# Kernel optimization log

Measured on AMD Instinct MI355X. Metric: run time of the kernel, lower is better.

Reference implementation:

```python
import jax, jax.numpy as jnp
import numpy as np
from jax import lax

T, B = 32, 16
NUM_ACTIONS = 18
HID = 256
C_V, C_K, C_S, NQ = 120, 8, 64, 4
NKEY, NVAL = C_K + C_S, C_V + C_S
Hh, Ww = 27, 20


def _spatial_basis():
    # Fourier spatial basis from Mott et al.; U = V = 8 -> 64 channels.
    h, w, U = Hh, Ww, 8
    p_h = np.arange(1, h + 1)[:, None] * np.ones((1, w)) * (np.pi / h)
    p_w = np.ones((h, 1)) * np.arange(1, w + 1)[None, :] * (np.pi / w)
    u = np.arange(1, U + 1)
    a = np.cos(p_h[:, :, None] * u)  # (h,w,8)
    b = np.cos(p_w[:, :, None] * u)  # (h,w,8)
    S = np.einsum('hwu,hwv->hwuv', a, b).reshape(h, w, U * U)
    return jnp.asarray(S, jnp.float32)

_S = _spatial_basis()


def _conv(x, w, b, stride, pad):
    y = lax.conv_general_dilated(x, w, stride, pad,
                                 dimension_numbers=('NCHW', 'OIHW', 'NCHW'))
    return y + b[None, :, None, None]


def setup_inputs() -> dict:
    key = jax.random.key(0)
    ks = iter(jax.random.split(key, 40))
    f32 = jnp.float32
    def rn(shape, s=0.05):
        return jax.random.normal(next(ks), shape, dtype=f32) * s
    return dict(
        frame=jax.random.normal(next(ks), (T, B, 3, 210, 160), dtype=f32),
        done=jnp.zeros((T, B), dtype=bool),
        last_action=jax.random.randint(next(ks), (T, B), 0, NUM_ACTIONS),
        reward=jax.random.normal(next(ks), (T, B), dtype=f32),
        core_h=jnp.zeros((B, HID), f32), core_c=jnp.zeros((B, HID), f32),
        conv_h=jnp.zeros((B, HID // 2, Hh, Ww), f32),
        conv_c=jnp.zeros((B, HID // 2, Hh, Ww), f32),
        cnn_w1=rn((32, 3, 8, 8)), cnn_b1=rn((32,)),
        cnn_w2=rn((64, 32, 4, 4)), cnn_b2=rn((64,)),
        lstm_w=rn((512, 192, 3, 3)), lstm_b=rn((512,)),
        qw1=rn((HID, 128)), qb1=rn((128,)),
        qw2=rn((128, NQ * NKEY)), qb2=rn((NQ * NKEY,)),
        qw3=rn((NQ * NKEY, NQ * NKEY)), qb3=rn((NQ * NKEY,)),
        aw1=rn((NVAL * NQ + NKEY * NQ + 1 + NUM_ACTIONS, 2 * HID)), ab1=rn((2 * HID,)),
        aw2=rn((2 * HID, HID)), ab2=rn((HID,)),
        w_ih=rn((4 * HID, HID)), w_hh=rn((4 * HID, HID)),
        b_ih=rn((4 * HID,)), b_hh=rn((4 * HID,)),
        pw=rn((HID, NUM_ACTIONS)), pb=rn((NUM_ACTIONS,)),
        vw=rn((HID, 1)), vb=rn((1,)),
    )


def reference(frame, done, last_action, reward, core_h, core_c, conv_h, conv_c,
              cnn_w1, cnn_b1, cnn_w2, cnn_b2, lstm_w, lstm_b,
              qw1, qb1, qw2, qb2, qw3, qb3, aw1, ab1, aw2, ab2,
              w_ih, w_hh, b_ih, b_hh, pw, pb, vw, vb):
    x = frame.reshape(T * B, 3, 210, 160)
    x = _conv(x, cnn_w1, cnn_b1, (4, 4), [(1, 1), (2, 2)])
    x = _conv(x, cnn_w2, cnn_b2, (2, 2), [(2, 2), (1, 1)])  # (T*B,64,27,20)
    x = x.reshape(T, B, 64, Hh, Ww)
    nd = (~done).astype(jnp.float32)  # (T,B)

    def vis_step(carry, inp):
        h, c = carry
        x_t, nd_t = inp
        m = nd_t[:, None, None, None]
        h, c = m * h, m * c
        gates = _conv(jnp.concatenate([x_t, h], axis=1), lstm_w, lstm_b,
                      (1, 1), [(1, 1), (1, 1)])
        ai, af, ao, ag = jnp.split(gates, 4, axis=1)
        c = jax.nn.sigmoid(af) * c + jax.nn.sigmoid(ai) * jnp.tanh(ag)
        h = jax.nn.sigmoid(ao) * jnp.tanh(c)
        return (h, c), h

    (vh, vc), O = lax.scan(vis_step, (conv_h, conv_c), (x, nd))
    # Faithful to the original `.view(N, h, w, c)` (a reinterpret, not a transpose).
    O = O.reshape(T * B, Hh, Ww, 128)
    Sb = jnp.broadcast_to(_S, (T * B, Hh, Ww, C_S))
    K = jnp.concatenate([O[..., :C_K], Sb], axis=3).reshape(T, B, Hh, Ww, NKEY)
    V = jnp.concatenate([O[..., C_K:], Sb], axis=3).reshape(T, B, Hh, Ww, NVAL)

    a1h = jax.nn.one_hot(last_action, NUM_ACTIONS, dtype=jnp.float32)  # (T,B,A)
    r = jnp.clip(reward, -1.0, 1.0)[..., None]  # (T,B,1)

    def core_step(carry, inp):
        h, c = carry
        K_t, V_t, r_t, a_t, nd_t = inp
        q = jax.nn.relu(h @ qw1 + qb1)
        q = jax.nn.relu(q @ qw2 + qb2)
        q = (q @ qw3 + qb3).reshape(B, NQ, NKEY)
        A = jnp.einsum('bhwk,bqk->bhwq', K_t, q)
        A = jax.nn.softmax(A.reshape(B, Hh * Ww, NQ), axis=1).reshape(B, Hh, Ww, NQ)
        ans = jnp.einsum('bhwq,bhwv->bqv', A, V_t)  # (B,NQ,NVAL)
        answer = jnp.concatenate(
            [ans.reshape(B, -1), q.reshape(B, -1), r_t, a_t], axis=1)
        ci = jax.nn.relu(answer @ aw1 + ab1) @ aw2 + ab2
        m = nd_t[:, None]
        h, c = m * h, m * c
        gates = ci @ w_ih.T + b_ih + h @ w_hh.T + b_hh  # torch gate order i,f,g,o
        gi, gf, gg, go = jnp.split(gates, 4, axis=1)
        c = jax.nn.sigmoid(gf) * c + jax.nn.sigmoid(gi) * jnp.tanh(gg)
        h = jax.nn.sigmoid(go) * jnp.tanh(c)
        return (h, c), h

    (ch, cc), outs = lax.scan(core_step, (core_h, core_c), (K, V, r, a1h, nd))
    out = outs.reshape(T * B, HID)
    logits = out @ pw + pb
    values = out @ vw + vb
    action = jnp.argmax(logits, axis=1)  # eval-mode action selection
    return (logits.reshape(T, B, NUM_ACTIONS), values.reshape(T, B),
            action.reshape(T, B), ch, cc, vh, vc)
```

## Files before the change

kernel.cpp:

```cpp
#include <hip/hip_runtime.h>
#include <math.h>

#define T_ 32
#define B_ 16
#define NA 18
#define P_ 540

typedef __attribute__((ext_vector_type(8)))  short short8;
typedef __attribute__((ext_vector_type(16))) float f32x16;

__device__ __forceinline__ float sigm(float x){ return 1.0f/(1.0f+expf(-x)); }
__device__ __forceinline__ unsigned short f2bf(float f){
    unsigned u = __float_as_uint(f);
    u += 0x7fff + ((u>>16)&1u);
    return (unsigned short)(u>>16);
}
__device__ __forceinline__ float bfu(unsigned short u){ return __uint_as_float(((unsigned)u)<<16); }

__global__ __launch_bounds__(256) void conv1k(const float* __restrict__ frame,
                                              const float* __restrict__ w,
                                              const float* __restrict__ bias,
                                              unsigned short* __restrict__ c1pad){
    __shared__ float tile[6048];
    int bid = blockIdx.x;
    int n = bid / 26, oh = (bid % 26)*2;
    int tid = threadIdx.x;
    const float* fb = frame + (size_t)n*3*210*160;
    for (int s = tid; s < 6048; s += 256){
        int col = s % 168;
        int row = (s/168) % 12;
        int ic  = s / 2016;
        int iy = oh*4 - 1 + row;
        int ix = col - 2;
        float v = 0.f;
        if (iy >= 0 && iy < 210 && ix >= 0 && ix < 160) v = fb[ic*33600 + iy*160 + ix];
        tile[s] = v;
    }
    __syncthreads();
    int oc = tid & 31, grp = tid >> 5;
    float acc[10] = {0.f,0.f,0.f,0.f,0.f,0.f,0.f,0.f,0.f,0.f};
    const float* wb = w + oc*192;
    for (int ic=0; ic<3; ++ic){
        #pragma unroll
        for (int kh=0; kh<8; ++kh){
            const float* wr = wb + ic*64 + kh*8;
            float4 w0 = *((const float4*)wr);
            float4 w1 = *((const float4*)(wr+4));
            const float* rowA = tile + ic*2016 + kh*168 + grp*20;
            float r[24];
            *((float4*)(r+ 0)) = *((const float4*)(rowA+ 0));
            *((float4*)(r+ 4)) = *((const float4*)(rowA+ 4));
            *((float4*)(r+ 8)) = *((const float4*)(rowA+ 8));
            *((float4*)(r+12)) = *((const float4*)(rowA+12));
            *((float4*)(r+16)) = *((const float4*)(rowA+16));
            *((float4*)(r+20)) = *((const float4*)(rowA+20));
            #pragma unroll
            for (int o=0;o<5;++o){
                acc[o] += r[o*4+0]*w0.x + r[o*4+1]*w0.y + r[o*4+2]*w0.z + r[o*4+3]*w0.w
                        + r[o*4+4]*w1.x + r[o*4+5]*w1.y + r[o*4+6]*w1.z + r[o*4+7]*w1.w;
            }
            const float* rowB = rowA + 672;
            *((float4*)(r+ 0)) = *((const float4*)(rowB+ 0));
            *((float4*)(r+ 4)) = *((const float4*)(rowB+ 4));
            *((float4*)(r+ 8)) = *((const float4*)(rowB+ 8));
            *((float4*)(r+12)) = *((const float4*)(rowB+12));
            *((float4*)(r+16)) = *((const float4*)(rowB+16));
            *((float4*)(r+20)) = *((const float4*)(rowB+20));
            #pragma unroll
            for (int o=0;o<5;++o){
                acc[5+o] += r[o*4+0]*w0.x + r[o*4+1]*w0.y + r[o*4+2]*w0.z + r[o*4+3]*w0.w
                          + r[o*4+4]*w1.x + r[o*4+5]*w1.y + r[o*4+6]*w1.z + r[o*4+7]*w1.w;
            }
        }
    }
    float bi = bias[oc];
    unsigned short* ob = c1pad + ((size_t)(n*32 + oc)*56 + oh+2)*42 + 1;
    #pragma unroll
    for (int o=0;o<5;++o) ob[grp*5+o] = f2bf(acc[o] + bi);
    ob += 42;
    #pragma unroll
    for (int o=0;o<5;++o) ob[grp*5+o] = f2bf(acc[5+o] + bi);
}

__global__ void apack2k(const float* __restrict__ w2, unsigned short* __restrict__ ap){
    int idx = blockIdx.x*256 + threadIdx.x;
    if (idx >= 32768) return;
    int j = idx & 7;
    int lane = (idx>>3) & 63;
    int mt = (idx>>9) & 1;
    int ic = idx >> 10;
    int k = ((lane>>5)<<3) + j;
    int oc = mt*32 + (lane & 31);
    ap[idx] = f2bf(w2[((oc*32 + ic)<<4) + k]);
}

__global__ __launch_bounds__(256) void c2mfma(const unsigned short* __restrict__ c1pad,
                                              const unsigned short* __restrict__ apack2,
                                              const float* __restrict__ bias,
                                              unsigned short* __restrict__ xpad){
    __shared__ unsigned short p2[2][3072];
    __shared__ float bsm[64];
    int bid = blockIdx.x;
    int s = bid / 5;
    int n0 = (bid % 5) * 128;
    int tid = threadIdx.x;
    int wave = tid >> 6, lane = tid & 63;
    int khalf = (lane>>5) << 3;
    if (tid < 64) bsm[tid] = bias[tid];
    const unsigned short* cb = c1pad + (size_t)s*32*2352;

    int soff[8], swaddr[8];
    #pragma unroll
    for (int q=0;q<8;++q){
        int idx = q*256 + tid;
        int n = idx & 127, k = idx >> 7;
        int p = n0 + n; if (p > 539) p = 539;
        soff[q] = ((p/20)*2 + (k>>2))*42 + (p%20)*2 + (k&3);
        swaddr[q] = n*24 + k;
    }
    #pragma unroll
    for (int q=0;q<8;++q) p2[0][swaddr[q]] = cb[soff[q]];
    unsigned short rv[8];
    #pragma unroll
    for (int q=0;q<8;++q) rv[q] = cb[2352 + soff[q]];

    int mt = wave >> 1, ntb = (wave & 1) * 2;
    short8 acur = *((const short8*)(apack2 + ((size_t)mt*64 + lane)*8));
    short8 anxt;
    f32x16 acc[2];
    #pragma unroll
    for (int jj=0;jj<2;++jj)
        #pragma unroll
        for (int rg=0;rg<16;++rg) acc[jj][rg] = 0.f;
    __syncthreads();

    for (int c=0; c<32; ++c){
        int buf = c & 1;
        if (c < 31){
            #pragma unroll
            for (int q=0;q<8;++q) p2[buf^1][swaddr[q]] = rv[q];
        }
        if (c < 30){
            const unsigned short* src = cb + (size_t)(c+2)*2352;
            #pragma unroll
            for (int q=0;q<8;++q) rv[q] = src[soff[q]];
        }
        if (c < 31) anxt = *((const short8*)(apack2 + ((size_t)((c+1)*2 + mt)*64 + lane)*8));
        #pragma unroll
        for (int jj=0;jj<2;++jj){
            int n = (ntb+jj)*32 + (lane & 31);
            short8 bf = *((const short8*)(&p2[buf][n*24 + khalf]));
            acc[jj] = __builtin_amdgcn_mfma_f32_32x32x16_bf16(acur, bf, acc[jj], 0, 0, 0);
        }
        acur = anxt;
        __syncthreads();
    }
    #pragma unroll
    for (int jj=0;jj<2;++jj){
        int pos = n0 + (ntb+jj)*32 + (lane & 31);
        if (pos >= 540) continue;
        int y = pos/20, x = pos%20;
        unsigned short* op = xpad + (size_t)s*64*640 + (y+1)*22 + x + 1;
        #pragma unroll
        for (int rg=0; rg<16; ++rg){
            int oc = mt*32 + (rg & 3) + 8*(rg>>2) + 4*(lane>>5);
            op[(size_t)oc*640] = f2bf(acc[jj][rg] + bsm[oc]);
        }
    }
}

__global__ void sbasisk(float* __restrict__ S){
    int idx = blockIdx.x*256 + threadIdx.x;
    if (idx >= P_*64) return;
    int s = idx & 63, p = idx >> 6;
    int y = p/20, x = p%20;
    int u = s >> 3, v = s & 7;
    double a  = cos((double)((y+1)*(u+1)) * M_PI / 27.0);
    double bb = cos((double)((x+1)*(v+1)) * M_PI / 20.0);
    S[idx] = (float)(a*bb);
}

__global__ void packw4k(const float* __restrict__ in, unsigned short* __restrict__ out, int R, int C){
    int idx = blockIdx.x*256 + threadIdx.x;
    int r4cnt = (R+3)>>2;
    if (idx >= r4cnt*C*4) return;
    int j = idx & 3;
    int rc = idx >> 2;
    int c = rc % C;
    int r = (rc / C)*4 + j;
    out[idx] = (r < R) ? f2bf(in[(size_t)r*C + c]) : (unsigned short)0;
}
__global__ void packt4k(const float* __restrict__ in, unsigned short* __restrict__ out, int R, int C){
    int idx = blockIdx.x*256 + threadIdx.x;
    int r4cnt = (R+3)>>2;
    if (idx >= r4cnt*C*4) return;
    int j = idx & 3;
    int rc = idx >> 2;
    int c = rc % C;
    int r = (rc / C)*4 + j;
    out[idx] = (r < R) ? f2bf(in[(size_t)c*R + r]) : (unsigned short)0;
}

__global__ void apack9k(const float* __restrict__ lw, unsigned short* __restrict__ ap){
    int idx = blockIdx.x*256 + threadIdx.x;
    if (idx >= 884736) return;
    int j = idx & 7;
    int lane = (idx>>3) & 63;
    int mt = (idx>>9) & 15;
    int f  = idx >> 13;
    int tap = f / 12, c = f % 12;
    int ch = c*16 + ((lane>>5)<<3) + j;
    int oc = mt*32 + (lane & 31);
    ap[idx] = f2bf(lw[(size_t)oc*1728 + ch*9 + tap]);
}

__global__ void h0packk(const float* __restrict__ h0, unsigned short* __restrict__ hpad){
    int idx = blockIdx.x*256 + threadIdx.x;
    if (idx >= 16*128*540) return;
    int plane = idx / 540, p = idx % 540;
    hpad[(size_t)plane*640 + (p/20+1)*22 + (p%20) + 1] = f2bf(h0[idx]);
}

__global__ __launch_bounds__(512) void gvck(const unsigned short* __restrict__ xpad,
                                            const unsigned short* __restrict__ hrd,
                                            unsigned short* __restrict__ hwr,
                                            const unsigned short* __restrict__ apack,
                                            const float* __restrict__ lb,
                                            const unsigned char* __restrict__ done,
                                            float* __restrict__ vh, float* __restrict__ vc,
                                            unsigned short* __restrict__ hreA,
                                            const float* __restrict__ S,
                                            const unsigned short* __restrict__ pq1, const float* __restrict__ qb1,
                                            const unsigned short* __restrict__ pq2, const float* __restrict__ qb2,
                                            const unsigned short* __restrict__ pq3, const float* __restrict__ qb3,
                                            const unsigned short* __restrict__ pa1, const float* __restrict__ ab1,
                                            const unsigned short* __restrict__ pa2, const float* __restrict__ ab2,
                                            const unsigned short* __restrict__ pih, const unsigned short* __restrict__ phh,
                                            const float* __restrict__ bih, const float* __restrict__ bhh,
                                            const float* __restrict__ reward, const int* __restrict__ lact,
                                            float* __restrict__ hsb, float* __restrict__ csb,
                                            float* __restrict__ outs,
                                            int t){
    __shared__ __align__(16) unsigned char smraw[65536];
    int bid = blockIdx.x;
    int tid = threadIdx.x;

    if (bid < 288){
        if (t >= T_) return;
        unsigned short* sm = (unsigned short*)smraw;
        float* gsm = (float*)smraw;
        int b  = bid % 16;
        int r  = bid / 16;
        int nb = r % 9;
        int mh = r / 9;
        int wave = tid >> 6, lane = tid & 63;
        int khalf = (lane>>5) << 3;
        int n0 = nb * 64;
        int y0 = n0 / 20;
        bool dn = done[t*B_ + b];

        const unsigned short* xb = xpad + ((size_t)(t*B_ + b))*64*640;
        const unsigned short* hb = hrd + (size_t)b*128*640;

        for (int rr = tid; rr < 1152; rr += 512){
            int ch = rr / 6, r6 = rr % 6;
            int prow = y0 + r6;
            unsigned short* dst = sm + (r6*22)*200 + ch;
            if (prow <= 28 && !(dn && ch >= 64)){
                const unsigned short* srcp = (ch < 64) ? (xb + ch*640 + prow*22)
                                                       : (hb + (ch-64)*640 + prow*22);
                const unsigned int* s32 = (const unsigned int*)srcp;
                #pragma unroll
                for (int c2=0;c2<11;++c2){
                    unsigned int v = s32[c2];
                    dst[(2*c2)*200]   = (unsigned short)(v & 0xffffu);
                    dst[(2*c2+1)*200] = (unsigned short)(v >> 16);
                }
            } else {
                #pragma unroll
                for (int c2=0;c2<22;++c2) dst[c2*200] = 0;
            }
        }

        int mt = (wave>>1)*4 + mh*2 + (wave&1);
        int sb[2];
        #pragma unroll
        for (int jj=0;jj<2;++jj){
            int p = n0 + jj*32 + (lane & 31); if (p > 539) p = 539;
            sb[jj] = ((p/20) - y0)*22 + (p%20);
        }
        f32x16 acc[2];
        #pragma unroll
        for (int jj=0;jj<2;++jj)
            #pragma unroll
            for (int rg=0;rg<16;++rg) acc[jj][rg] = 0.f;
        __syncthreads();

        for (int tap=0; tap<9; ++tap){
            int tadd = (tap/3)*22 + (tap%3);
            #pragma unroll
            for (int c=0;c<12;++c){
                short8 af = *((const short8*)(apack + ((size_t)((tap*12+c)*16 + mt)*64 + lane)*8));
                int ch0 = c*16 + khalf;
                short8 b0 = *((const short8*)(&sm[(sb[0]+tadd)*200 + ch0]));
                short8 b1 = *((const short8*)(&sm[(sb[1]+tadd)*200 + ch0]));
                acc[0] = __builtin_amdgcn_mfma_f32_32x32x16_bf16(af, b0, acc[0], 0, 0, 0);
                acc[1] = __builtin_amdgcn_mfma_f32_32x32x16_bf16(af, b1, acc[1], 0, 0, 0);
            }
        }
        __syncthreads();

        int g8 = wave >> 1, ih = wave & 1;
        #pragma unroll
        for (int j=0;j<2;++j){
            int p_loc = j*32 + (lane & 31);
            #pragma unroll
            for (int rg=0; rg<16; ++rg){
                int c_loc = ih*32 + 4*(lane>>5) + (rg & 3) + 8*(rg>>2);
                gsm[g8*4096 + c_loc*64 + p_loc] = acc[j][rg];
            }
        }
        __syncthreads();

        {
            int p_loc = tid & 63, c0 = tid >> 6;
            int pg = n0 + p_loc;
            if (pg < 540){
                float m = dn ? 0.f : 1.f;
                int y = pg/20, x = pg%20;
                #pragma unroll
                for (int e=0;e<8;++e){
                    int c_loc = c0*8 + e;
                    int cg = mh*64 + c_loc;
                    float gi = gsm[        c_loc*64 + p_loc] + lb[      cg];
                    float gf = gsm[ 4096 + c_loc*64 + p_loc] + lb[128 + cg];
                    float go = gsm[ 8192 + c_loc*64 + p_loc] + lb[256 + cg];
                    float gg = gsm[12288 + c_loc*64 + p_loc] + lb[384 + cg];
                    size_t idx = ((size_t)b*128 + cg)*540 + pg;
                    float cold = vc[idx] * m;
                    float cn = sigm(gf)*cold + sigm(gi)*tanhf(gg);
                    float hn = sigm(go)*tanhf(cn);
                    vc[idx] = cn;
                    if (t == T_-1) vh[idx] = hn;
                    hwr[((size_t)b*128 + cg)*640 + (y+1)*22 + x + 1] = f2bf(hn);
                    int flat = cg*540 + pg;
                    int pos = (flat/2560)*20 + (flat/128)%20;
                    int ch  = flat & 127;
                    hreA[((size_t)(t*B_ + b)*540 + pos)*128 + ch] = f2bf(hn);
                }
            }
        }
        return;
    }

    if (t == 0) return;
    int tc = t - 1;
    int b = bid - 288;
    float* fs = (float*)smraw;
    float* hs   = fs;
    float* cs   = fs + 256;
    float* hs2  = fs + 512;
    float* q1   = fs + 768;
    float* q2   = fs + 896;
    float* q3   = fs + 1184;
    float* elog = fs + 1472;
    float* red  = fs + 3632;
    float* ansv = fs + 3664;
    float* hid  = fs + 4720;
    float* cis  = fs + 5232;
    float* gb   = fs + 5488;

    if (tid < 256){ hs[tid] = hsb[b*256+tid]; cs[tid] = csb[b*256+tid]; }
    if (tid >= 256 && tid < 269) ansv[1043 + (tid-256)] = 0.f;
    __syncthreads();

    float m = done[tc*B_+b] ? 0.f : 1.f;
    if (tid < 128){
        float a0=0.f,a1=0.f,a2=0.f,a3=0.f;
        for (int i4=0;i4<64;++i4){
            ushort4 w = *((const ushort4*)(pq1 + (size_t)((i4<<7)+tid)*4));
            float4 h4 = *((const float4*)(hs + i4*4));
            a0 += h4.x*bfu(w.x); a1 += h4.y*bfu(w.y);
            a2 += h4.z*bfu(w.z); a3 += h4.w*bfu(w.w);
        }
        q1[tid] = fmaxf(qb1[tid] + ((a0+a1)+(a2+a3)), 0.f);
    }
    __syncthreads();
    if (tid < 288){
        float a0=0.f,a1=0.f,a2=0.f,a3=0.f;
        for (int i4=0;i4<32;++i4){
            ushort4 w = *((const ushort4*)(pq2 + (size_t)(i4*288+tid)*4));
            float4 h4 = *((const float4*)(q1 + i4*4));
            a0 += h4.x*bfu(w.x); a1 += h4.y*bfu(w.y);
            a2 += h4.z*bfu(w.z); a3 += h4.w*bfu(w.w);
        }
        q2[tid] = fmaxf(qb2[tid] + ((a0+a1)+(a2+a3)), 0.f);
    }
    __syncthreads();
    if (tid < 288){
        float a0=0.f,a1=0.f,a2=0.f,a3=0.f;
        for (int i4=0;i4<72;++i4){
            ushort4 w = *((const ushort4*)(pq3 + (size_t)(i4*288+tid)*4));
            float4 h4 = *((const float4*)(q2 + i4*4));
            a0 += h4.x*bfu(w.x); a1 += h4.y*bfu(w.y);
            a2 += h4.z*bfu(w.z); a3 += h4.w*bfu(w.w);
        }
        float a = qb3[tid] + ((a0+a1)+(a2+a3));
        q3[tid] = a;
        ansv[736+tid] = a;
    }
    if (tid == 0){ float r = reward[tc*B_+b]; ansv[1024] = fminf(1.f,fmaxf(-1.f,r)); }
    if (tid >= 32 && tid < 32+NA) ansv[1025 + tid-32] = (lact[tc*B_+b] == tid-32) ? 1.f : 0.f;
    __syncthreads();

    const unsigned short* hrb = hreA + (size_t)(tc*B_ + b)*540*128;
    for (int idx = tid; idx < 4*P_; idx += 512){
        int qi = idx / P_, p = idx % P_;
        const unsigned short* hp = hrb + (size_t)p*128;
        uint4 hv = *((const uint4*)hp);
        const float* qv = q3 + qi*72;
        float a = __uint_as_float(hv.x<<16)*qv[0] + __uint_as_float(hv.x & 0xffff0000u)*qv[1]
                + __uint_as_float(hv.y<<16)*qv[2] + __uint_as_float(hv.y & 0xffff0000u)*qv[3]
                + __uint_as_float(hv.z<<16)*qv[4] + __uint_as_float(hv.z & 0xffff0000u)*qv[5]
                + __uint_as_float(hv.w<<16)*qv[6] + __uint_as_float(hv.w & 0xffff0000u)*qv[7];
        const float* Sp = S + p*64;
        #pragma unroll
        for (int s2=0;s2<16;++s2){
            float4 sv = *((const float4*)(Sp + 4*s2));
            a += sv.x*qv[8+4*s2] + sv.y*qv[9+4*s2] + sv.z*qv[10+4*s2] + sv.w*qv[11+4*s2];
        }
        elog[qi*P_ + p] = a;
    }
    __syncthreads();
    {
        int qi = tid >> 7, lt = tid & 127;
        float mx = -1e30f;
        for (int p = lt; p < P_; p += 128) mx = fmaxf(mx, elog[qi*P_ + p]);
        for (int off=32; off; off>>=1) mx = fmaxf(mx, __shfl_down(mx, off));
        if ((tid & 63) == 0) red[tid>>6] = mx;
        __syncthreads();
        if (tid < 4) red[16+tid] = fmaxf(red[2*tid], red[2*tid+1]);
        __syncthreads();
        mx = red[16+qi];
        float sm = 0.f;
        for (int p = lt; p < P_; p += 128){ float e = expf(elog[qi*P_ + p]-mx); elog[qi*P_ + p] = e; sm += e; }
        for (int off=32; off; off>>=1) sm += __shfl_down(sm, off);
        if ((tid & 63) == 0) red[8 + (tid>>6)] = sm;
        __syncthreads();
        if (tid < 4) red[24+tid] = red[8+2*tid] + red[8+2*tid+1];
        __syncthreads();
    }
    if (tid < 240){
        int g = tid >> 2;
        int qi = g / 15, vb = g % 15;
        int pc = tid & 3;
        float ac[8] = {0,0,0,0,0,0,0,0};
        const unsigned short* hb8 = hrb + 8 + vb*8;
        for (int p = pc*135; p < pc*135+135; ++p){
            float e = elog[qi*P_ + p];
            uint4 hv = *((const uint4*)(hb8 + (size_t)p*128));
            ac[0] += e*__uint_as_float(hv.x<<16);
            ac[1] += e*__uint_as_float(hv.x & 0xffff0000u);
            ac[2] += e*__uint_as_float(hv.y<<16);
            ac[3] += e*__uint_as_float(hv.y & 0xffff0000u);
            ac[4] += e*__uint_as_float(hv.z<<16);
            ac[5] += e*__uint_as_float(hv.z & 0xffff0000u);
            ac[6] += e*__uint_as_float(hv.w<<16);
            ac[7] += e*__uint_as_float(hv.w & 0xffff0000u);
        }
        #pragma unroll
        for (int j=0;j<8;++j){ ac[j] += __shfl_down(ac[j],2); ac[j] += __shfl_down(ac[j],1); }
        if ((tid&3)==0){
            float inv2 = 1.f/red[24+qi];
            #pragma unroll
            for (int j=0;j<8;++j) ansv[qi*184 + vb*8 + j] = ac[j]*inv2;
        }
    } else if (tid < 496){
        int u = tid - 240;
        int g = u >> 2;
        int qi = g >> 4, vb4 = g & 15;
        int pc = u & 3;
        float ac[4] = {0,0,0,0};
        const float* Sp = S + vb4*4;
        for (int p = pc*135; p < pc*135+135; ++p){
            float e = elog[qi*P_ + p];
            float4 sv = *((const float4*)(Sp + (size_t)p*64));
            ac[0]+=e*sv.x; ac[1]+=e*sv.y; ac[2]+=e*sv.z; ac[3]+=e*sv.w;
        }
        #pragma unroll
        for (int j=0;j<4;++j){ ac[j] += __shfl_down(ac[j],2); ac[j] += __shfl_down(ac[j],1); }
        if ((tid&3)==0){
            float inv2 = 1.f/red[24+qi];
            #pragma unroll
            for (int j=0;j<4;++j) ansv[qi*184 + 120 + vb4*4 + j] = ac[j]*inv2;
        }
    }
    __syncthreads();
    {
        float a0=ab1[tid], a1=0.f, a2=0.f, a3=0.f;
        for (int i4=0;i4<261;++i4){
            ushort4 w = *((const ushort4*)(pa1 + (size_t)((i4<<9)+tid)*4));
            float4 av = *((const float4*)(ansv + i4*4));
            a0 += av.x*bfu(w.x); a1 += av.y*bfu(w.y);
            a2 += av.z*bfu(w.z); a3 += av.w*bfu(w.w);
        }
        hid[tid] = fmaxf((a0+a1)+(a2+a3), 0.f);
    }
    if (tid < 256) hs2[tid] = hs[tid]*m;
    __syncthreads();
    if (tid < 256){
        float a0=ab2[tid],a1=0.f,a2=0.f,a3=0.f;
        for (int i4=0;i4<128;++i4){
            ushort4 w = *((const ushort4*)(pa2 + (size_t)((i4<<8)+tid)*4));
            float4 hv = *((const float4*)(hid + i4*4));
            a0 += hv.x*bfu(w.x); a1 += hv.y*bfu(w.y);
            a2 += hv.z*bfu(w.z); a3 += hv.w*bfu(w.w);
        }
        cis[tid] = (a0+a1)+(a2+a3);
    }
    __syncthreads();
    for (int g = tid; g < 1024; g += 512){
        float a0=bih[g]+bhh[g], a1=0.f, a2=0.f, a3=0.f;
        for (int i4=0;i4<64;++i4){
            ushort4 wi = *((const ushort4*)(pih + (size_t)((i4<<10)+g)*4));
            ushort4 wh = *((const ushort4*)(phh + (size_t)((i4<<10)+g)*4));
            float4 cv = *((const float4*)(cis + i4*4));
            float4 hv = *((const float4*)(hs2 + i4*4));
            a0 += cv.x*bfu(wi.x) + hv.x*bfu(wh.x);
            a1 += cv.y*bfu(wi.y) + hv.y*bfu(wh.y);
            a2 += cv.z*bfu(wi.z) + hv.z*bfu(wh.z);
            a3 += cv.w*bfu(wi.w) + hv.w*bfu(wh.w);
        }
        gb[g] = (a0+a1)+(a2+a3);
    }
    __syncthreads();
    if (tid < 256){
        float gi = gb[tid], gf = gb[256+tid], gg = gb[512+tid], go = gb[768+tid];
        float cold = cs[tid]*m;
        float cn = sigm(gf)*cold + sigm(gi)*tanhf(gg);
        float hn = sigm(go)*tanhf(cn);
        csb[b*256+tid] = cn;
        hsb[b*256+tid] = hn;
        outs[(tc*B_+b)*256+tid] = hn;
    }
}

__global__ __launch_bounds__(64) void finalk(const float* __restrict__ outs,
                                             const float* __restrict__ pw, const float* __restrict__ pb,
                                             const float* __restrict__ vw, const float* __restrict__ vb,
                                             float* __restrict__ dout){
    int row = blockIdx.x, tid = threadIdx.x;
    __shared__ float os[256];
    __shared__ float lg[NA];
    for (int i=tid; i<256; i+=64) os[i] = outs[row*256+i];
    __syncthreads();
    if (tid < NA){
        float a = pb[tid];
        for (int i=0;i<256;++i) a += os[i]*pw[i*NA+tid];
        lg[tid] = a;
        dout[row*NA + tid] = a;
    } else if (tid == 32){
        float a = vb[0];
        for (int i=0;i<256;++i) a += os[i]*vw[i];
        dout[9216 + row] = a;
    }
    __syncthreads();
    if (tid == 0){
        int am = 0; float bv = lg[0];
        for (int j=1;j<NA;++j) if (lg[j] > bv){ bv = lg[j]; am = j; }
        dout[9728 + row] = (float)am;
    }
}

extern "C" void kernel_launch(void* const* d_in, const int* in_sizes, int n_in,
                              void* d_out, int out_size, void* d_ws, size_t ws_size,
                              hipStream_t stream) {
    const float* frame   = (const float*)d_in[0];
    const unsigned char* done = (const unsigned char*)d_in[1];
    const int*   lact    = (const int*)d_in[2];
    const float* reward  = (const float*)d_in[3];
    const float* core_h0 = (const float*)d_in[4];
    const float* core_c0 = (const float*)d_in[5];
    const float* conv_h0 = (const float*)d_in[6];
    const float* conv_c0 = (const float*)d_in[7];
    const float* cnn_w1  = (const float*)d_in[8];
    const float* cnn_b1  = (const float*)d_in[9];
    const float* cnn_w2  = (const float*)d_in[10];
    const float* cnn_b2  = (const float*)d_in[11];
    const float* lstm_w  = (const float*)d_in[12];
    const float* lstm_b  = (const float*)d_in[13];
    const float* qw1 = (const float*)d_in[14]; const float* qb1 = (const float*)d_in[15];
    const float* qw2 = (const float*)d_in[16]; const float* qb2 = (const float*)d_in[17];
    const float* qw3 = (const float*)d_in[18]; const float* qb3 = (const float*)d_in[19];
    const float* aw1 = (const float*)d_in[20]; const float* ab1 = (const float*)d_in[21];
    const float* aw2 = (const float*)d_in[22]; const float* ab2 = (const float*)d_in[23];
    const float* w_ih = (const float*)d_in[24]; const float* w_hh = (const float*)d_in[25];
    const float* b_ih = (const float*)d_in[26]; const float* b_hh = (const float*)d_in[27];
    const float* pw = (const float*)d_in[28]; const float* pb = (const float*)d_in[29];
    const float* vw = (const float*)d_in[30]; const float* vb = (const float*)d_in[31];

    float* ws = (float*)d_ws;
    float* dout = (float*)d_out;

    unsigned short* xpad   = (unsigned short*)ws;
    unsigned short* c1pad  = (unsigned short*)(ws + 10485760);
    unsigned short* hreA   = (unsigned short*)(ws + 10485760);
    unsigned short* apack  = (unsigned short*)(ws + 28180480);
    unsigned short* wpk    = (unsigned short*)(ws + 28966912);
    unsigned short* pq1 = wpk;
    unsigned short* pq2 = wpk + 32768;
    unsigned short* pq3 = wpk + 69632;
    unsigned short* pa1 = wpk + 152576;
    unsigned short* pa2 = wpk + 687104;
    unsigned short* pih = wpk + 818176;
    unsigned short* phh = wpk + 1080320;
    unsigned short* hpad0  = (unsigned short*)(ws + 29753344);
    unsigned short* apack2 = (unsigned short*)(ws + 30408704);
    unsigned short* hpad1  = (unsigned short*)(ws + 30425088);
    float* hsb   = ws + 31080448;
    float* csb   = ws + 31084544;
    float* vh    = ws + 34881536;
    float* vc    = ws + 35987456;
    float* S     = ws + 37093376;
    float* outs  = ws + 37127936;

    hipMemsetAsync(xpad,  0, (size_t)20971520*2, stream);
    hipMemsetAsync(c1pad, 0, (size_t)38535168*2, stream);

    apack2k<<<128, 256, 0, stream>>>(cnn_w2, apack2);
    conv1k<<<512*26, 256, 0, stream>>>(frame, cnn_w1, cnn_b1, c1pad);
    c2mfma<<<2560, 256, 0, stream>>>(c1pad, apack2, cnn_b2, xpad);

    hipMemsetAsync(hpad0, 0, (size_t)1310720*2, stream);
    hipMemsetAsync(hpad1, 0, (size_t)1310720*2, stream);
    sbasisk<<<135, 256, 0, stream>>>(S);
    apack9k<<<3456, 256, 0, stream>>>(lstm_w, apack);
    packw4k<<<128,  256, 0, stream>>>(qw1, pq1, 256, 128);
    packw4k<<<144,  256, 0, stream>>>(qw2, pq2, 128, 288);
    packw4k<<<324,  256, 0, stream>>>(qw3, pq3, 288, 288);
    packw4k<<<2088, 256, 0, stream>>>(aw1, pa1, 1043, 512);
    packw4k<<<512,  256, 0, stream>>>(aw2, pa2, 512, 256);
    packt4k<<<1024, 256, 0, stream>>>(w_ih, pih, 256, 1024);
    packt4k<<<1024, 256, 0, stream>>>(w_hh, phh, 256, 1024);
    h0packk<<<4320, 256, 0, stream>>>(conv_h0, hpad0);
    hipMemcpyAsync(vc,  conv_c0, (size_t)16*128*540*sizeof(float), hipMemcpyDeviceToDevice, stream);
    hipMemcpyAsync(hsb, core_h0, (size_t)16*256*sizeof(float), hipMemcpyDeviceToDevice, stream);
    hipMemcpyAsync(csb, core_c0, (size_t)16*256*sizeof(float), hipMemcpyDeviceToDevice, stream);

    for (int t = 0; t <= T_; ++t){
        gvck<<<304, 512, 0, stream>>>(xpad, (t&1)?hpad1:hpad0, (t&1)?hpad0:hpad1,
                                      apack, lstm_b, done, vh, vc, hreA,
                                      S, pq1,qb1,pq2,qb2,pq3,qb3,
                                      pa1,ab1,pa2,ab2, pih,phh,b_ih,b_hh,
                                      reward, lact, hsb, csb, outs, t);
    }

    finalk<<<512, 64, 0, stream>>>(outs, pw, pb, vw, vb, dout);

    hipMemcpyAsync(dout + 10240,   outs + (size_t)31*B_*256, (size_t)16*256*sizeof(float), hipMemcpyDeviceToDevice, stream);
    hipMemcpyAsync(dout + 14336,   csb, (size_t)16*256*sizeof(float), hipMemcpyDeviceToDevice, stream);
    hipMemcpyAsync(dout + 18432,   vh,  (size_t)16*128*540*sizeof(float), hipMemcpyDeviceToDevice, stream);
    hipMemcpyAsync(dout + 1124352, vc,  (size_t)16*128*540*sizeof(float), hipMemcpyDeviceToDevice, stream);
}
```

Baseline: 4.929 ms.

## Switch conv-LSTM inputs to channel-last layout and read B fragments directly from global

The conv2 output and the recurrent hidden state now use a position-major, channel-contiguous layout instead of padded planar planes. The gate conv kernel drops its shared-memory staging and barriers, loading MFMA B fragments straight from global memory with per-tap bounds masks for the zero padding. It skips the hidden-state half of the reduction when done is set, and reorders blocks so the core-LSTM blocks come first. This removes the staging copy, the padded-buffer memsets and the syncthreads, at the cost of more uncached global loads per MFMA that now rely on L2/L1 reuse.

```diff
diff --git a/kernel.cpp b/kernel.cpp
--- a/kernel.cpp
+++ b/kernel.cpp
@@ -97,7 +97,7 @@
 __global__ __launch_bounds__(256) void c2mfma(const unsigned short* __restrict__ c1pad,
                                               const unsigned short* __restrict__ apack2,
                                               const float* __restrict__ bias,
-                                              unsigned short* __restrict__ xpad){
+                                              unsigned short* __restrict__ xre){
     __shared__ unsigned short p2[2][3072];
     __shared__ float bsm[64];
     int bid = blockIdx.x;
@@ -159,12 +159,11 @@
     for (int jj=0;jj<2;++jj){
         int pos = n0 + (ntb+jj)*32 + (lane & 31);
         if (pos >= 540) continue;
-        int y = pos/20, x = pos%20;
-        unsigned short* op = xpad + (size_t)s*64*640 + (y+1)*22 + x + 1;
+        unsigned short* op = xre + ((size_t)s*540 + pos)*64;
         #pragma unroll
         for (int rg=0; rg<16; ++rg){
             int oc = mt*32 + (rg & 3) + 8*(rg>>2) + 4*(lane>>5);
-            op[(size_t)oc*640] = f2bf(acc[jj][rg] + bsm[oc]);
+            op[oc] = f2bf(acc[jj][rg] + bsm[oc]);
         }
     }
 }
@@ -214,16 +213,18 @@
     ap[idx] = f2bf(lw[(size_t)oc*1728 + ch*9 + tap]);
 }
 
-__global__ void h0packk(const float* __restrict__ h0, unsigned short* __restrict__ hpad){
+__global__ void h0rek(const float* __restrict__ h0, unsigned short* __restrict__ h0re){
     int idx = blockIdx.x*256 + threadIdx.x;
     if (idx >= 16*128*540) return;
     int plane = idx / 540, p = idx % 540;
-    hpad[(size_t)plane*640 + (p/20+1)*22 + (p%20) + 1] = f2bf(h0[idx]);
-}
-
-__global__ __launch_bounds__(512) void gvck(const unsigned short* __restrict__ xpad,
+    int b = plane >> 7, c = plane & 127;
+    h0re[((size_t)b*540 + p)*128 + c] = f2bf(h0[idx]);
+}
+
+__global__ __launch_bounds__(512) void gvck(const unsigned short* __restrict__ xre,
                                             const unsigned short* __restrict__ hrd,
                                             unsigned short* __restrict__ hwr,
+                                            const unsigned short* __restrict__ h0re,
                                             const unsigned short* __restrict__ apack,
                                             const float* __restrict__ lb,
                                             const unsigned char* __restrict__ done,
@@ -245,70 +246,69 @@
     int bid = blockIdx.x;
     int tid = threadIdx.x;
 
-    if (bid < 288){
+    if (bid >= 16){
         if (t >= T_) return;
-        unsigned short* sm = (unsigned short*)smraw;
         float* gsm = (float*)smraw;
-        int b  = bid % 16;
-        int r  = bid / 16;
+        int vb = bid - 16;
+        int b  = vb % 16;
+        int r  = vb / 16;
         int nb = r % 9;
         int mh = r / 9;
         int wave = tid >> 6, lane = tid & 63;
         int khalf = (lane>>5) << 3;
         int n0 = nb * 64;
-        int y0 = n0 / 20;
         bool dn = done[t*B_ + b];
 
-        const unsigned short* xb = xpad + ((size_t)(t*B_ + b))*64*640;
-        const unsigned short* hb = hrd + (size_t)b*128*640;
-
-        for (int rr = tid; rr < 1152; rr += 512){
-            int ch = rr / 6, r6 = rr % 6;
-            int prow = y0 + r6;
-            unsigned short* dst = sm + (r6*22)*200 + ch;
-            if (prow <= 28 && !(dn && ch >= 64)){
-                const unsigned short* srcp = (ch < 64) ? (xb + ch*640 + prow*22)
-                                                       : (hb + (ch-64)*640 + prow*22);
-                const unsigned int* s32 = (const unsigned int*)srcp;
-                #pragma unroll
-                for (int c2=0;c2<11;++c2){
-                    unsigned int v = s32[c2];
-                    dst[(2*c2)*200]   = (unsigned short)(v & 0xffffu);
-                    dst[(2*c2+1)*200] = (unsigned short)(v >> 16);
-                }
-            } else {
-                #pragma unroll
-                for (int c2=0;c2<22;++c2) dst[c2*200] = 0;
-            }
-        }
+        const unsigned short* xb = xre + (size_t)(t*B_ + b)*540*64;
+        const unsigned short* hp2 = (t==0) ? (h0re + (size_t)b*540*128)
+                                           : (hrd  + (size_t)b*540*128);
 
         int mt = (wave>>1)*4 + mh*2 + (wave&1);
-        int sb[2];
+
+        int poff[2][9]; int vmask[2][9];
         #pragma unroll
         for (int jj=0;jj<2;++jj){
             int p = n0 + jj*32 + (lane & 31); if (p > 539) p = 539;
-            sb[jj] = ((p/20) - y0)*22 + (p%20);
-        }
+            int y = p/20, x = p%20;
+            #pragma unroll
+            for (int tap=0;tap<9;++tap){
+                int dy = tap/3 - 1, dx = tap%3 - 1;
+                int yy = y+dy, xx = x+dx;
+                vmask[jj][tap] = ((unsigned)yy < 27u) && ((unsigned)xx < 20u);
+                poff[jj][tap] = yy*20 + xx;
+            }
+        }
+        const short8 z8 = {0,0,0,0,0,0,0,0};
         f32x16 acc[2];
         #pragma unroll
         for (int jj=0;jj<2;++jj)
             #pragma unroll
             for (int rg=0;rg<16;++rg) acc[jj][rg] = 0.f;
-        __syncthreads();
-
-        for (int tap=0; tap<9; ++tap){
-            int tadd = (tap/3)*22 + (tap%3);
-            #pragma unroll
-            for (int c=0;c<12;++c){
+
+        for (int c=0;c<4;++c){
+            int cho = c*16 + khalf;
+            #pragma unroll
+            for (int tap=0;tap<9;++tap){
                 short8 af = *((const short8*)(apack + ((size_t)((tap*12+c)*16 + mt)*64 + lane)*8));
-                int ch0 = c*16 + khalf;
-                short8 b0 = *((const short8*)(&sm[(sb[0]+tadd)*200 + ch0]));
-                short8 b1 = *((const short8*)(&sm[(sb[1]+tadd)*200 + ch0]));
+                short8 b0 = vmask[0][tap] ? *((const short8*)(xb + poff[0][tap]*64 + cho)) : z8;
+                short8 b1 = vmask[1][tap] ? *((const short8*)(xb + poff[1][tap]*64 + cho)) : z8;
                 acc[0] = __builtin_amdgcn_mfma_f32_32x32x16_bf16(af, b0, acc[0], 0, 0, 0);
                 acc[1] = __builtin_amdgcn_mfma_f32_32x32x16_bf16(af, b1, acc[1], 0, 0, 0);
             }
         }
-        __syncthreads();
+        if (!dn){
+            for (int c=4;c<12;++c){
+                int cho = (c-4)*16 + khalf;
+                #pragma unroll
+                for (int tap=0;tap<9;++tap){
+                    short8 af = *((const short8*)(apack + ((size_t)((tap*12+c)*16 + mt)*64 + lane)*8));
+                    short8 b0 = vmask[0][tap] ? *((const short8*)(hp2 + poff[0][tap]*128 + cho)) : z8;
+                    short8 b1 = vmask[1][tap] ? *((const short8*)(hp2 + poff[1][tap]*128 + cho)) : z8;
+                    acc[0] = __builtin_amdgcn_mfma_f32_32x32x16_bf16(af, b0, acc[0], 0, 0, 0);
+                    acc[1] = __builtin_amdgcn_mfma_f32_32x32x16_bf16(af, b1, acc[1], 0, 0, 0);
+                }
+            }
+        }
 
         int g8 = wave >> 1, ih = wave & 1;
         #pragma unroll
@@ -327,7 +327,6 @@
             int pg = n0 + p_loc;
             if (pg < 540){
                 float m = dn ? 0.f : 1.f;
-                int y = pg/20, x = pg%20;
                 #pragma unroll
                 for (int e=0;e<8;++e){
                     int c_loc = c0*8 + e;
@@ -342,11 +341,12 @@
                     float hn = sigm(go)*tanhf(cn);
                     vc[idx] = cn;
                     if (t == T_-1) vh[idx] = hn;
-                    hwr[((size_t)b*128 + cg)*640 + (y+1)*22 + x + 1] = f2bf(hn);
+                    unsigned short hb16 = f2bf(hn);
+                    hwr[((size_t)b*540 + pg)*128 + cg] = hb16;
                     int flat = cg*540 + pg;
                     int pos = (flat/2560)*20 + (flat/128)%20;
                     int ch  = flat & 127;
-                    hreA[((size_t)(t*B_ + b)*540 + pos)*128 + ch] = f2bf(hn);
+                    hreA[((size_t)(t*B_ + b)*540 + pos)*128 + ch] = hb16;
                 }
             }
         }
@@ -355,7 +355,7 @@
 
     if (t == 0) return;
     int tc = t - 1;
-    int b = bid - 288;
+    int b = bid;
     float* fs = (float*)smraw;
     float* hs   = fs;
     float* cs   = fs + 256;
@@ -602,7 +602,7 @@
     float* ws = (float*)d_ws;
     float* dout = (float*)d_out;
 
-    unsigned short* xpad   = (unsigned short*)ws;
+    unsigned short* xre    = (unsigned short*)ws;
     unsigned short* c1pad  = (unsigned short*)(ws + 10485760);
     unsigned short* hreA   = (unsigned short*)(ws + 10485760);
     unsigned short* apack  = (unsigned short*)(ws + 28180480);
@@ -614,25 +614,23 @@
     unsigned short* pa2 = wpk + 687104;
     unsigned short* pih = wpk + 818176;
     unsigned short* phh = wpk + 1080320;
-    unsigned short* hpad0  = (unsigned short*)(ws + 29753344);
+    unsigned short* h0re   = (unsigned short*)(ws + 29753344);
     unsigned short* apack2 = (unsigned short*)(ws + 30408704);
-    unsigned short* hpad1  = (unsigned short*)(ws + 30425088);
+    unsigned short* hpl0   = (unsigned short*)(ws + 30425088);
     float* hsb   = ws + 31080448;
     float* csb   = ws + 31084544;
+    unsigned short* hpl1   = (unsigned short*)(ws + 31100928);
     float* vh    = ws + 34881536;
     float* vc    = ws + 35987456;
     float* S     = ws + 37093376;
     float* outs  = ws + 37127936;
 
-    hipMemsetAsync(xpad,  0, (size_t)20971520*2, stream);
     hipMemsetAsync(c1pad, 0, (size_t)38535168*2, stream);
 
     apack2k<<<128, 256, 0, stream>>>(cnn_w2, apack2);
     conv1k<<<512*26, 256, 0, stream>>>(frame, cnn_w1, cnn_b1, c1pad);
-    c2mfma<<<2560, 256, 0, stream>>>(c1pad, apack2, cnn_b2, xpad);
-
-    hipMemsetAsync(hpad0, 0, (size_t)1310720*2, stream);
-    hipMemsetAsync(hpad1, 0, (size_t)1310720*2, stream);
+    c2mfma<<<2560, 256, 0, stream>>>(c1pad, apack2, cnn_b2, xre);
+
     sbasisk<<<135, 256, 0, stream>>>(S);
     apack9k<<<3456, 256, 0, stream>>>(lstm_w, apack);
     packw4k<<<128,  256, 0, stream>>>(qw1, pq1, 256, 128);
@@ -642,13 +640,14 @@
     packw4k<<<512,  256, 0, stream>>>(aw2, pa2, 512, 256);
     packt4k<<<1024, 256, 0, stream>>>(w_ih, pih, 256, 1024);
     packt4k<<<1024, 256, 0, stream>>>(w_hh, phh, 256, 1024);
-    h0packk<<<4320, 256, 0, stream>>>(conv_h0, hpad0);
+    h0rek<<<4320, 256, 0, stream>>>(conv_h0, h0re);
     hipMemcpyAsync(vc,  conv_c0, (size_t)16*128*540*sizeof(float), hipMemcpyDeviceToDevice, stream);
     hipMemcpyAsync(hsb, core_h0, (size_t)16*256*sizeof(float), hipMemcpyDeviceToDevice, stream);
     hipMemcpyAsync(csb, core_c0, (size_t)16*256*sizeof(float), hipMemcpyDeviceToDevice, stream);
 
     for (int t = 0; t <= T_; ++t){
-        gvck<<<304, 512, 0, stream>>>(xpad, (t&1)?hpad1:hpad0, (t&1)?hpad0:hpad1,
+        gvck<<<304, 512, 0, stream>>>(xre,
+                                      (t&1)?hpl0:hpl1, (t&1)?hpl1:hpl0, h0re,
                                       apack, lstm_b, done, vh, vc, hreA,
                                       S, pq1,qb1,pq2,qb2,pq3,qb3,
                                       pa1,ab1,pa2,ab2, pih,phh,b_ih,b_hh,
```

Result: faster. 4.801 ms (-2.6%).
